# Performance work log

Hardware: AMD Instinct MI355X
Metric: run time of the kernel (lower is better)

The kernel has to match this reference:

```python
import jax, jax.numpy as jnp
import numpy as np

N_NODES = 50000
N_EDGES = 800000
N_GRAPHS = 64
F0 = 64          # num_features
HID = 512        # hidden_size
N_OUT = 1


def setup_inputs() -> dict:
    key = jax.random.key(0)
    ks = jax.random.split(key, 16)

    def p(k, shape, scale):
        return jax.random.normal(k, shape, jnp.float32) * scale

    inp = {}
    inp["feature"] = jax.random.normal(ks[0], (N_NODES, F0), jnp.float32)
    inp["edge_index"] = jax.random.randint(ks[1], (2, N_EDGES), 0, N_NODES)
    inp["protein_batch"] = jnp.sort(jax.random.randint(ks[2], (N_NODES,), 0, N_GRAPHS))

    dims = [(F0, F0), (F0, 2 * F0), (2 * F0, 4 * F0)]
    for i, (din, dout) in enumerate(dims):
        s = 1.0 / np.sqrt(din)
        inp[f"W{i+1}"] = p(ks[3 + 3 * i], (din, dout), s)      # GATConv lin weight
        inp[f"att{i+1}"] = p(ks[4 + 3 * i], (2, dout), 0.1)    # [att_src; att_dst]
        inp[f"b{i+1}"] = jnp.zeros((dout,), jnp.float32)       # GATConv bias
    inp["fc1_w"] = p(ks[12], (4 * F0, HID), 1.0 / np.sqrt(4 * F0))
    inp["fc1_b"] = jnp.zeros((HID,), jnp.float32)
    inp["fc2_w"] = p(ks[13], (HID, N_OUT), 1.0 / np.sqrt(HID))
    inp["fc2_b"] = jnp.zeros((N_OUT,), jnp.float32)
    return inp


def _gat_conv(x, src, dst, W, att, b):
    """PyG GATConv, heads=1, concat=True, negative_slope=0.2 (self-loops already in src/dst)."""
    h = x @ W                                             # [N, Dout]
    # per-edge attention logit: a_src . h_j + a_dst . h_i
    alpha = jax.nn.leaky_relu(h @ att[0], 0.2 * 0 + 0.0)  # placeholder, replaced below
    logit = jax.nn.leaky_relu((h @ att[0])[src] + (h @ att[1])[dst], negative_slope=0.2)  # [E]
    # segment softmax over edges grouped by destination node
    m = jax.ops.segment_max(logit, dst, num_segments=N_NODES)      # [N]
    e = jnp.exp(logit - m[dst])                                    # [E]
    s = jax.ops.segment_sum(e, dst, num_segments=N_NODES)          # [N]
    coef = e / s[dst]                                              # [E]
    out = jax.ops.segment_sum(coef[:, None] * h[src], dst, num_segments=N_NODES)  # [N, Dout]
    return out + b


def reference(feature, edge_index, protein_batch,
              W1, att1, b1, W2, att2, b2, W3, att3, b3,
              fc1_w, fc1_b, fc2_w, fc2_b):
    loop = jnp.arange(N_NODES)
    src = jnp.concatenate([edge_index[0], loop])   # add_self_loops=True
    dst = jnp.concatenate([edge_index[1], loop])

    x = jax.nn.relu(_gat_conv(feature, src, dst, W1, att1, b1))
    x = jax.nn.relu(_gat_conv(x, src, dst, W2, att2, b2))
    x = jax.nn.relu(_gat_conv(x, src, dst, W3, att3, b3))

    # global mean pool per graph
    sums = jax.ops.segment_sum(x, protein_batch, num_segments=N_GRAPHS)          # [G, 4F]
    cnts = jax.ops.segment_sum(jnp.ones((N_NODES,), x.dtype), protein_batch,
                               num_segments=N_GRAPHS)                            # [G]
    gc = sums / jnp.maximum(cnts, 1.0)[:, None]

    gc = jax.nn.relu(gc @ fc1_w + fc1_b)   # dropout is identity at inference
    return gc @ fc2_w + fc2_b
```

## Files before the change

### kernel.cpp

```cpp
#include <hip/hip_runtime.h>
#include <hip/hip_bf16.h>

#define N_NODES 50000
#define N_EDGES 800000
#define E_TOT   850000
#define N_GRAPHS 64
#define HID 512
#define NBC 196
#define PB  304
#define EB  3321
#define WB  12500

typedef unsigned short u16;
typedef __attribute__((ext_vector_type(8))) short short8;
typedef __attribute__((ext_vector_type(4))) float floatx4;
typedef union { uint4 u; short8 s; } frag_u;

__device__ inline unsigned f2b(float x) {
    unsigned u = __float_as_uint(x);
    return (u + 0x7fffu + ((u >> 16) & 1u)) >> 16;
}
__device__ inline float b2f_lo(unsigned u) { return __uint_as_float(u << 16); }
__device__ inline float b2f_hi(unsigned u) { return __uint_as_float(u & 0xffff0000u); }

struct PrepDesc {
    const float* W[3];
    const float* att[3];
    float* wsd[3];
    u16* Wt[3];
};

__global__ __launch_bounds__(256) void prep_count_kernel(PrepDesc d,
                                                         const int* __restrict__ dst_e,
                                                         int* __restrict__ cnt,
                                                         int* __restrict__ order) {
    const int DIN[3]  = {64, 64, 128};
    const int DOUT[3] = {64, 128, 256};
    int b = blockIdx.x;
    if (b >= PB) {
        int e = (b - PB) * 256 + threadIdx.x;
        if (e >= E_TOT) return;
        int dd = (e < N_EDGES) ? dst_e[e] : (e - N_EDGES);
        order[e] = atomicAdd(&cnt[dd], 1);
        return;
    }
    if (b < 128) {
        int wg = (b * 256 + (int)threadIdx.x) >> 6;
        int lane = threadIdx.x & 63;
        int l = (wg < 128) ? 0 : (wg < 256) ? 1 : 2;
        int base = (l == 0) ? 0 : (l == 1) ? 128 : 256;
        int k = wg - base;
        int Din = DIN[l], Dout = DOUT[l];
        int half = (k >= Din) ? 1 : 0;
        int row = half ? (k - Din) : k;
        float s = 0.f;
        for (int j = lane; j < Dout; j += 64)
            s += d.W[l][(size_t)row * Dout + j] * d.att[l][half * Dout + j];
#pragma unroll
        for (int off = 32; off > 0; off >>= 1) s += __shfl_xor(s, off);
        if (lane == 0) d.wsd[l][k] = s;
    } else {
        int t = (b - 128) * 256 + (int)threadIdx.x;
        int l; int off;
        if (t < 4096)       { l = 0; off = t; }
        else if (t < 12288) { l = 1; off = t - 4096; }
        else if (t < 45056) { l = 2; off = t - 12288; }
        else return;
        int Din = DIN[l], Dout = DOUT[l];
        int row = off / Dout, j = off & (Dout - 1);
        d.Wt[l][(size_t)j * Din + row] = (u16)f2b(d.W[l][off]);
    }
}

__global__ __launch_bounds__(256) void scan_cvt_kernel(const int* __restrict__ cnt,
                                                       int* __restrict__ row_ptr,
                                                       int* __restrict__ blocksum,
                                                       const float* __restrict__ feature,
                                                       const float* __restrict__ wsd1,
                                                       u16* __restrict__ Fb,
                                                       float* __restrict__ lsld1) {
    if (blockIdx.x < NBC) {
        __shared__ int buf[256];
        int tid = threadIdx.x;
        int i = blockIdx.x * 256 + tid;
        int v = (i < N_NODES) ? cnt[i] : 0;
        buf[tid] = v;
        __syncthreads();
        for (int off = 1; off < 256; off <<= 1) {
            int t = (tid >= off) ? buf[tid - off] : 0;
            __syncthreads();
            buf[tid] += t;
            __syncthreads();
        }
        if (i < N_NODES) row_ptr[i] = buf[tid] - v;
        if (tid == 255) blocksum[blockIdx.x] = buf[255];
    } else {
        int wid = ((blockIdx.x - NBC) * 256 + (int)threadIdx.x) >> 6;
        int lane = threadIdx.x & 63;
        if (wid >= N_NODES) return;
        float h = feature[(size_t)wid * 64 + lane];
        float a0 = h * wsd1[lane];
        float a1 = h * wsd1[64 + lane];
#pragma unroll
        for (int off = 32; off > 0; off >>= 1) {
            a0 += __shfl_xor(a0, off);
            a1 += __shfl_xor(a1, off);
        }
        if (lane == 0) { lsld1[wid] = a0; lsld1[N_NODES + wid] = a1; }
        Fb[(size_t)wid * 64 + lane] = (u16)f2b(h);
    }
}

__global__ __launch_bounds__(256) void scan_block_kernel(const int* __restrict__ blocksum,
                                                         int* __restrict__ blockoff,
                                                         int* __restrict__ row_ptr2_last) {
    __shared__ int buf[256];
    int tid = threadIdx.x;
    int v = (tid < NBC) ? blocksum[tid] : 0;
    buf[tid] = v;
    __syncthreads();
    for (int off = 1; off < 256; off <<= 1) {
        int t = (tid >= off) ? buf[tid - off] : 0;
        __syncthreads();
        buf[tid] += t;
        __syncthreads();
    }
    blockoff[tid] = buf[tid] - v;
    if (tid == 255) *row_ptr2_last = buf[255];
}

__global__ __launch_bounds__(256) void fin_fill_kernel(const int* __restrict__ edge_index,
                                                       const int* __restrict__ row_ptr,
                                                       const int* __restrict__ blockoff,
                                                       const int* __restrict__ order,
                                                       int* __restrict__ col_idx,
                                                       int* __restrict__ row_ptr2) {
    if (blockIdx.x < NBC) {
        int i = blockIdx.x * 256 + threadIdx.x;
        if (i < N_NODES) row_ptr2[i] = row_ptr[i] + blockoff[blockIdx.x];
        return;
    }
    int e = (blockIdx.x - NBC) * 256 + threadIdx.x;
    if (e >= E_TOT) return;
    int s, d;
    if (e < N_EDGES) { s = edge_index[e]; d = edge_index[N_EDGES + e]; }
    else             { s = e - N_EDGES;   d = s; }
    col_idx[row_ptr[d] + blockoff[d >> 8] + order[e]] = s;
}

template <int NN, int KK>
__global__ __launch_bounds__(256) void sgemm_mfma_kernel(const u16* __restrict__ A,
                                                         const u16* __restrict__ Bt,
                                                         u16* __restrict__ C,
                                                         const float* __restrict__ bias,
                                                         const float* __restrict__ wsd_next,
                                                         float* __restrict__ lsld_next,
                                                         const int* __restrict__ batch,
                                                         float* __restrict__ gsum_pool,
                                                         int M) {
    constexpr int NT = 4;
    constexpr int KSTEPS = KK / 32;
    constexpr int CS = 72;
    __shared__ u16 cst[4][32 * CS];
    const int lane = threadIdx.x & 63;
    const int w = threadIdx.x >> 6;
    const int c = lane & 15;
    const int q = lane >> 4;
    const int bn = blockIdx.y * 64;
    const int r0 = blockIdx.x * 128 + w * 32;
    int ar0 = r0 + c;      if (ar0 > M - 1) ar0 = M - 1;
    int ar1 = r0 + 16 + c; if (ar1 > M - 1) ar1 = M - 1;
    const u16* __restrict__ Ap0 = A + (size_t)ar0 * KK + q * 8;
    const u16* __restrict__ Ap1 = A + (size_t)ar1 * KK + q * 8;
    floatx4 acc[2][NT];
#pragma unroll
    for (int i = 0; i < 2; ++i)
#pragma unroll
        for (int b = 0; b < NT; ++b) acc[i][b] = (floatx4){0.f, 0.f, 0.f, 0.f};
#pragma unroll
    for (int ks = 0; ks < KSTEPS; ++ks) {
        const int k0 = ks * 32;
        frag_u a0, a1, bf[NT];
        a0.u = *(const uint4*)(Ap0 + k0);
        a1.u = *(const uint4*)(Ap1 + k0);
#pragma unroll
        for (int b = 0; b < NT; ++b)
            bf[b].u = *(const uint4*)(Bt + (size_t)(bn + b * 16 + c) * KK + q * 8 + k0);
#pragma unroll
        for (int b = 0; b < NT; ++b) {
            acc[0][b] = __builtin_amdgcn_mfma_f32_16x16x32_bf16(a0.s, bf[b].s, acc[0][b], 0, 0, 0);
            acc[1][b] = __builtin_amdgcn_mfma_f32_16x16x32_bf16(a1.s, bf[b].s, acc[1][b], 0, 0, 0);
        }
    }

    if (gsum_pool) {
        float bsv[NT];
#pragma unroll
        for (int b = 0; b < NT; ++b) bsv[b] = bias[bn + b * 16 + c];
        const bool full = (r0 + 31 < M);
        const int rl = full ? (r0 + 31) : (M - 1);
        if (full && batch[r0] == batch[rl]) {
            const int gr = batch[r0];
#pragma unroll
            for (int b = 0; b < NT; ++b) {
                float s = 0.f;
#pragma unroll
                for (int i = 0; i < 2; ++i)
#pragma unroll
                    for (int g = 0; g < 4; ++g) s += fmaxf(acc[i][b][g] + bsv[b], 0.f);
                s += __shfl_xor(s, 16);
                s += __shfl_xor(s, 32);
                if (q == 0) atomicAdd(&gsum_pool[gr * 256 + bn + b * 16 + c], s);
            }
        } else {
#pragma unroll
            for (int i = 0; i < 2; ++i) {
                int curg = -1;
                float sb[NT] = {0.f, 0.f, 0.f, 0.f};
#pragma unroll
                for (int g = 0; g < 4; ++g) {
                    int r = r0 + i * 16 + q * 4 + g;
                    if (r < M) {
                        int gr = batch[r];
                        if (gr != curg) {
                            if (curg >= 0) {
#pragma unroll
                                for (int b = 0; b < NT; ++b) {
                                    atomicAdd(&gsum_pool[curg * 256 + bn + b * 16 + c], sb[b]);
                                    sb[b] = 0.f;
                                }
                            }
                            curg = gr;
                        }
#pragma unroll
                        for (int b = 0; b < NT; ++b) sb[b] += fmaxf(acc[i][b][g] + bsv[b], 0.f);
                    }
                }
                if (curg >= 0) {
#pragma unroll
                    for (int b = 0; b < NT; ++b)
                        atomicAdd(&gsum_pool[curg * 256 + bn + b * 16 + c], sb[b]);
                }
            }
        }
        return;
    }

    const bool has_next = (wsd_next != nullptr);
    u16* __restrict__ cb = cst[w];
    float ps[2][4] = {}, pd[2][4] = {};
#pragma unroll
    for (int b = 0; b < NT; ++b) {
        const int col = bn + b * 16 + c;
        const float bsv = bias[col];
        const float wsv = has_next ? wsd_next[col] : 0.f;
        const float wdv = has_next ? wsd_next[NN + col] : 0.f;
#pragma unroll
        for (int i = 0; i < 2; ++i) {
#pragma unroll
            for (int g = 0; g < 4; ++g) {
                float v = fmaxf(acc[i][b][g] + bsv, 0.f);
                cb[(i * 16 + q * 4 + g) * CS + b * 16 + c] = (u16)f2b(v);
                ps[i][g] += v * wsv;
                pd[i][g] += v * wdv;
            }
        }
    }
    if (has_next) {
#pragma unroll
        for (int i = 0; i < 2; ++i)
#pragma unroll
            for (int g = 0; g < 4; ++g) {
#pragma unroll
                for (int mm = 1; mm < 16; mm <<= 1) {
                    ps[i][g] += __shfl_xor(ps[i][g], mm);
                    pd[i][g] += __shfl_xor(pd[i][g], mm);
                }
            }
        if (c == 0) {
#pragma unroll
            for (int i = 0; i < 2; ++i)
#pragma unroll
                for (int g = 0; g < 4; ++g) {
                    int r = r0 + i * 16 + q * 4 + g;
                    if (r < M) {
                        atomicAdd(&lsld_next[r], ps[i][g]);
                        atomicAdd(&lsld_next[M + r], pd[i][g]);
                    }
                }
        }
    }
#pragma unroll
    for (int p = 0; p < 4; ++p) {
        int lr = p * 8 + (lane >> 3);
        int r = r0 + lr;
        if (r < M) {
            uint4 val = *(const uint4*)&cb[lr * CS + (lane & 7) * 8];
            *(uint4*)(C + (size_t)r * NN + bn + (lane & 7) * 8) = val;
        }
    }
}

template <int D>
__global__ __launch_bounds__(256) void gather_fused_kernel(const u16* __restrict__ X,
                                                           const float* __restrict__ lsld,
                                                           const int* __restrict__ row_ptr,
                                                           const int* __restrict__ col_idx,
                                                           u16* __restrict__ out) {
    constexpr int L = D / 8;
    constexpr int P = 64 / L;
    __shared__ float2 ec_all[4][64];
    int wid = (blockIdx.x * 256 + threadIdx.x) >> 6;
    int lane = threadIdx.x & 63;
    if (wid >= N_NODES) return;
    float2* __restrict__ ec = ec_all[threadIdx.x >> 6];
    const int start = row_ptr[wid];
    const int end = row_ptr[wid + 1];
    const int deg = end - start;
    const float ldi = lsld[N_NODES + wid];
    const float* __restrict__ ls = lsld;
    const int eslot = lane / L;
    const int fidx = lane % L;
    float a[8] = {0.f, 0.f, 0.f, 0.f, 0.f, 0.f, 0.f, 0.f};

    auto fma8 = [&](float cc, uint4 v) {
        a[0] += cc * b2f_lo(v.x); a[1] += cc * b2f_hi(v.x);
        a[2] += cc * b2f_lo(v.y); a[3] += cc * b2f_hi(v.y);
        a[4] += cc * b2f_lo(v.z); a[5] += cc * b2f_hi(v.z);
        a[6] += cc * b2f_lo(v.w); a[7] += cc * b2f_hi(v.w);
    };

    if (deg <= 64) {
        int srcl = 0;
        float l = -3.0e38f;
        if (lane < deg) {
            srcl = col_idx[start + lane];
            float t = ls[srcl] + ldi;
            l = (t > 0.f) ? t : 0.2f * t;
        }
        float m = l;
#pragma unroll
        for (int off = 32; off > 0; off >>= 1) m = fmaxf(m, __shfl_xor(m, off));
        float e = (lane < deg) ? __expf(l - m) : 0.f;
        float s = e;
#pragma unroll
        for (int off = 32; off > 0; off >>= 1) s += __shfl_xor(s, off);
        ec[lane] = make_float2(e / s, __int_as_float(srcl));

        const int nsteps = (deg + P - 1) / P;
        for (int g0 = 0; g0 < nsteps; g0 += 4) {
            float2 p[4]; uint4 v[4];
#pragma unroll
            for (int j = 0; j < 4; ++j) {
                int idx = (g0 + j) * P + eslot;
                bool valid = idx < deg;
                p[j] = ec[valid ? idx : 0];
                if (!valid) p[j].x = 0.f;
            }
#pragma unroll
            for (int j = 0; j < 4; ++j)
                v[j] = *(const uint4*)(X + (size_t)__float_as_int(p[j].y) * D + fidx * 8);
#pragma unroll
            for (int j = 0; j < 4; ++j) fma8(p[j].x, v[j]);
        }
    } else {
        float m = -3.0e38f;
        for (int e = start + lane; e < end; e += 64) {
            float t = ls[col_idx[e]] + ldi;
            t = (t > 0.f) ? t : 0.2f * t;
            m = fmaxf(m, t);
        }
#pragma unroll
        for (int off = 32; off > 0; off >>= 1) m = fmaxf(m, __shfl_xor(m, off));
        float ssum = 0.f;
        for (int e = start + lane; e < end; e += 64) {
            float t = ls[col_idx[e]] + ldi;
            t = (t > 0.f) ? t : 0.2f * t;
            ssum += __expf(t - m);
        }
#pragma unroll
        for (int off = 32; off > 0; off >>= 1) ssum += __shfl_xor(ssum, off);
        const float inv = 1.0f / ssum;
        for (int e0 = start; e0 < end; e0 += P) {
            int e = e0 + eslot;
            if (e < end) {
                int src = col_idx[e];
                float t = ls[src] + ldi;
                t = (t > 0.f) ? t : 0.2f * t;
                float cc = __expf(t - m) * inv;
                uint4 v = *(const uint4*)(X + (size_t)src * D + fidx * 8);
                fma8(cc, v);
            }
        }
    }
#pragma unroll
    for (int mm = L; mm < 64; mm <<= 1) {
#pragma unroll
        for (int i = 0; i < 8; ++i) a[i] += __shfl_xor(a[i], mm);
    }
    if (lane < L) {
        uint4 o;
        o.x = f2b(a[0]) | (f2b(a[1]) << 16);
        o.y = f2b(a[2]) | (f2b(a[3]) << 16);
        o.z = f2b(a[4]) | (f2b(a[5]) << 16);
        o.w = f2b(a[6]) | (f2b(a[7]) << 16);
        *(uint4*)(out + (size_t)wid * D + lane * 8) = o;
    }
}

__device__ inline int lower_bound_dev(const int* __restrict__ a, int n, int v) {
    int lo = 0, hi = n;
    while (lo < hi) { int mid = (lo + hi) >> 1; if (a[mid] < v) lo = mid + 1; else hi = mid; }
    return lo;
}

__global__ __launch_bounds__(256) void fc_kernel(const float* __restrict__ gsum,
                                                 const int* __restrict__ batch,
                                                 const float* __restrict__ w1,
                                                 const float* __restrict__ b1,
                                                 const float* __restrict__ w2,
                                                 const float* __restrict__ b2,
                                                 float* __restrict__ out) {
    __shared__ float gc[256];
    __shared__ float h1s[HID];
    __shared__ float red[256];
    __shared__ int s_cnt;
    int g = blockIdx.x;
    int tid = threadIdx.x;
    if (tid == 0)
        s_cnt = lower_bound_dev(batch, N_NODES, g + 1) - lower_bound_dev(batch, N_NODES, g);
    __syncthreads();
    float denom = fmaxf((float)s_cnt, 1.0f);
    gc[tid] = gsum[g * 256 + tid] / denom;
    __syncthreads();
#pragma unroll
    for (int jj = 0; jj < 2; ++jj) {
        int j = tid + jj * 256;
        float sum = b1[j];
        for (int k = 0; k < 256; ++k) sum += gc[k] * w1[k * HID + j];
        h1s[j] = (sum > 0.f) ? sum : 0.f;
    }
    __syncthreads();
    float acc = h1s[tid] * w2[tid] + h1s[tid + 256] * w2[tid + 256];
    red[tid] = acc;
    __syncthreads();
    for (int off = 128; off > 0; off >>= 1) {
        if (tid < off) red[tid] += red[tid + off];
        __syncthreads();
    }
    if (tid == 0) out[g] = red[0] + b2[0];
}

extern "C" void kernel_launch(void* const* d_in, const int* in_sizes, int n_in,
                              void* d_out, int out_size, void* d_ws, size_t ws_size,
                              hipStream_t stream) {
    const float* feature  = (const float*)d_in[0];
    const int*   edge_idx = (const int*)d_in[1];
    const int*   batch    = (const int*)d_in[2];
    const float* W1    = (const float*)d_in[3];
    const float* att1  = (const float*)d_in[4];
    const float* b1    = (const float*)d_in[5];
    const float* W2    = (const float*)d_in[6];
    const float* att2  = (const float*)d_in[7];
    const float* b2    = (const float*)d_in[8];
    const float* W3    = (const float*)d_in[9];
    const float* att3  = (const float*)d_in[10];
    const float* b3    = (const float*)d_in[11];
    const float* fc1_w = (const float*)d_in[12];
    const float* fc1_b = (const float*)d_in[13];
    const float* fc2_w = (const float*)d_in[14];
    const float* fc2_b = (const float*)d_in[15];
    float* out = (float*)d_out;

    char* w = (char*)d_ws;
    auto alloc = [&](size_t bytes) {
        char* p = w;
        w += (bytes + 255) & ~(size_t)255;
        return p;
    };
    u16* Fb    = (u16*)alloc((size_t)N_NODES * 64 * 2);
    u16* X1b   = (u16*)alloc((size_t)N_NODES * 64 * 2);
    u16* X2b   = (u16*)alloc((size_t)N_NODES * 128 * 2);
    u16* AGGb  = (u16*)alloc((size_t)N_NODES * 128 * 2);
    float* lsld1 = (float*)alloc((size_t)N_NODES * 2 * 4);
    char* zbase = w;
    int* cnt      = (int*)alloc((size_t)N_NODES * 4);
    float* gsum   = (float*)alloc(64 * 256 * 4);
    float* lsld23 = (float*)alloc((size_t)N_NODES * 4 * 4);
    size_t zbytes = (size_t)(w - zbase);
    float* lsld2 = lsld23;
    float* lsld3 = lsld23 + (size_t)N_NODES * 2;
    float* wsd1  = (float*)alloc(2 * 64 * 4);
    float* wsd2  = (float*)alloc(2 * 64 * 4);
    float* wsd3  = (float*)alloc(2 * 128 * 4);
    u16* Wt1   = (u16*)alloc(64 * 64 * 2);
    u16* Wt2   = (u16*)alloc(128 * 64 * 2);
    u16* Wt3   = (u16*)alloc(256 * 128 * 2);
    int* row_ptr  = (int*)alloc((size_t)N_NODES * 4);
    int* row_ptr2 = (int*)alloc((size_t)(N_NODES + 1) * 4);
    int* col_idx  = (int*)alloc((size_t)E_TOT * 4);
    int* order    = (int*)alloc((size_t)E_TOT * 4);
    int* blocksum = (int*)alloc(256 * 4);
    int* blockoff = (int*)alloc(256 * 4);

    hipMemsetAsync(zbase, 0, zbytes, stream);

    const int GB = (N_NODES + 127) / 128;

    PrepDesc pd;
    pd.W[0] = W1; pd.W[1] = W2; pd.W[2] = W3;
    pd.att[0] = att1; pd.att[1] = att2; pd.att[2] = att3;
    pd.wsd[0] = wsd1; pd.wsd[1] = wsd2; pd.wsd[2] = wsd3;
    pd.Wt[0] = Wt1; pd.Wt[1] = Wt2; pd.Wt[2] = Wt3;

    prep_count_kernel<<<PB + EB, 256, 0, stream>>>(pd, edge_idx + N_EDGES, cnt, order);
    scan_cvt_kernel<<<NBC + WB, 256, 0, stream>>>(cnt, row_ptr, blocksum, feature, wsd1, Fb, lsld1);
    scan_block_kernel<<<1, 256, 0, stream>>>(blocksum, blockoff, row_ptr2 + N_NODES);
    fin_fill_kernel<<<NBC + EB, 256, 0, stream>>>(edge_idx, row_ptr, blockoff, order, col_idx, row_ptr2);

    gather_fused_kernel<64><<<WB, 256, 0, stream>>>(Fb, lsld1, row_ptr2, col_idx, AGGb);
    sgemm_mfma_kernel<64, 64><<<dim3(GB, 1), 256, 0, stream>>>(AGGb, Wt1, X1b, b1, wsd2, lsld2, nullptr, nullptr, N_NODES);

    gather_fused_kernel<64><<<WB, 256, 0, stream>>>(X1b, lsld2, row_ptr2, col_idx, AGGb);
    sgemm_mfma_kernel<128, 64><<<dim3(GB, 2), 256, 0, stream>>>(AGGb, Wt2, X2b, b2, wsd3, lsld3, nullptr, nullptr, N_NODES);

    gather_fused_kernel<128><<<WB, 256, 0, stream>>>(X2b, lsld3, row_ptr2, col_idx, AGGb);
    sgemm_mfma_kernel<256, 128><<<dim3(GB, 4), 256, 0, stream>>>(AGGb, Wt3, nullptr, b3, nullptr, nullptr, batch, gsum, N_NODES);

    fc_kernel<<<N_GRAPHS, 256, 0, stream>>>(gsum, batch, fc1_w, fc1_b, fc2_w, fc2_b, out);
}
```

Baseline: 299.8 us.

## Fuse block scan into fill kernel and use two nodes per wave for D=64 gathers

Every block of the fill kernel now redoes the small 196-entry block-offset scan in shared memory, which removes the separate single-block scan launch and its blockoff buffer. A new gather2 kernel handles two destination nodes per 64-lane wave for the 64-wide feature layers, with 32 lanes per node covering 4 edges by 8 bf16 features. This is meant to reduce idle lanes and halve the number of waves for low-degree nodes. The cost is redundant scan work in every fill block and more shuffle reductions for the per-node sums.

Measured after the change: 289.8 us, median of 2. -3.4%, faster.

```diff
diff --git a/kernel.cpp b/kernel.cpp
--- a/kernel.cpp
+++ b/kernel.cpp
@@ -10,6 +10,7 @@
 #define PB  304
 #define EB  3321
 #define WB  12500
+#define WB2 6250
 
 typedef unsigned short u16;
 typedef __attribute__((ext_vector_type(8))) short short8;
@@ -111,10 +112,14 @@
     }
 }
 
-__global__ __launch_bounds__(256) void scan_block_kernel(const int* __restrict__ blocksum,
-                                                         int* __restrict__ blockoff,
-                                                         int* __restrict__ row_ptr2_last) {
+__global__ __launch_bounds__(256) void fin_fill_kernel(const int* __restrict__ edge_index,
+                                                       const int* __restrict__ row_ptr,
+                                                       const int* __restrict__ blocksum,
+                                                       const int* __restrict__ order,
+                                                       int* __restrict__ col_idx,
+                                                       int* __restrict__ row_ptr2) {
     __shared__ int buf[256];
+    __shared__ int boff[256];
     int tid = threadIdx.x;
     int v = (tid < NBC) ? blocksum[tid] : 0;
     buf[tid] = v;
@@ -125,27 +130,21 @@
         buf[tid] += t;
         __syncthreads();
     }
-    blockoff[tid] = buf[tid] - v;
-    if (tid == 255) *row_ptr2_last = buf[255];
-}
-
-__global__ __launch_bounds__(256) void fin_fill_kernel(const int* __restrict__ edge_index,
-                                                       const int* __restrict__ row_ptr,
-                                                       const int* __restrict__ blockoff,
-                                                       const int* __restrict__ order,
-                                                       int* __restrict__ col_idx,
-                                                       int* __restrict__ row_ptr2) {
+    boff[tid] = buf[tid] - v;
+    __syncthreads();
+
     if (blockIdx.x < NBC) {
-        int i = blockIdx.x * 256 + threadIdx.x;
-        if (i < N_NODES) row_ptr2[i] = row_ptr[i] + blockoff[blockIdx.x];
+        int i = blockIdx.x * 256 + tid;
+        if (i < N_NODES) row_ptr2[i] = row_ptr[i] + boff[blockIdx.x];
+        if (blockIdx.x == 0 && tid == NBC - 1) row_ptr2[N_NODES] = buf[tid];
         return;
     }
-    int e = (blockIdx.x - NBC) * 256 + threadIdx.x;
+    int e = (blockIdx.x - NBC) * 256 + tid;
     if (e >= E_TOT) return;
     int s, d;
     if (e < N_EDGES) { s = edge_index[e]; d = edge_index[N_EDGES + e]; }
     else             { s = e - N_EDGES;   d = s; }
-    col_idx[row_ptr[d] + blockoff[d >> 8] + order[e]] = s;
+    col_idx[row_ptr[d] + boff[d >> 8] + order[e]] = s;
 }
 
 template <int NN, int KK>
@@ -298,6 +297,113 @@
             uint4 val = *(const uint4*)&cb[lr * CS + (lane & 7) * 8];
             *(uint4*)(C + (size_t)r * NN + bn + (lane & 7) * 8) = val;
         }
+    }
+}
+
+__global__ __launch_bounds__(256) void gather2_kernel(const u16* __restrict__ X,
+                                                      const float* __restrict__ lsld,
+                                                      const int* __restrict__ row_ptr,
+                                                      const int* __restrict__ col_idx,
+                                                      u16* __restrict__ out) {
+    __shared__ float2 ec_all[4][64];
+    int gw = (blockIdx.x * 256 + threadIdx.x) >> 6;
+    int lane = threadIdx.x & 63;
+    int half = lane >> 5;
+    int hl = lane & 31;
+    int nid = gw * 2 + half;
+    if (nid >= N_NODES) return;
+    float2* __restrict__ ec = ec_all[threadIdx.x >> 6] + half * 32;
+    const int start = row_ptr[nid];
+    const int end = row_ptr[nid + 1];
+    const int deg = end - start;
+    const float ldi = lsld[N_NODES + nid];
+    const float* __restrict__ ls = lsld;
+    const int eslot = hl >> 3;
+    const int fidx = hl & 7;
+    float a[8] = {0.f, 0.f, 0.f, 0.f, 0.f, 0.f, 0.f, 0.f};
+
+    auto fma8 = [&](float cc, uint4 v) {
+        a[0] += cc * b2f_lo(v.x); a[1] += cc * b2f_hi(v.x);
+        a[2] += cc * b2f_lo(v.y); a[3] += cc * b2f_hi(v.y);
+        a[4] += cc * b2f_lo(v.z); a[5] += cc * b2f_hi(v.z);
+        a[6] += cc * b2f_lo(v.w); a[7] += cc * b2f_hi(v.w);
+    };
+
+    if (deg <= 32) {
+        int srcl = 0;
+        float l = -3.0e38f;
+        if (hl < deg) {
+            srcl = col_idx[start + hl];
+            float t = ls[srcl] + ldi;
+            l = (t > 0.f) ? t : 0.2f * t;
+        }
+        float m = l;
+#pragma unroll
+        for (int off = 16; off > 0; off >>= 1) m = fmaxf(m, __shfl_xor(m, off));
+        float e = (hl < deg) ? __expf(l - m) : 0.f;
+        float s = e;
+#pragma unroll
+        for (int off = 16; off > 0; off >>= 1) s += __shfl_xor(s, off);
+        ec[hl] = make_float2(e / s, __int_as_float(srcl));
+
+        const int nsteps = (deg + 3) >> 2;
+        for (int g0 = 0; g0 < nsteps; g0 += 4) {
+            float2 p[4]; uint4 v[4];
+#pragma unroll
+            for (int j = 0; j < 4; ++j) {
+                int idx = (g0 + j) * 4 + eslot;
+                bool valid = idx < deg;
+                p[j] = ec[valid ? idx : 0];
+                if (!valid) p[j].x = 0.f;
+            }
+#pragma unroll
+            for (int j = 0; j < 4; ++j)
+                v[j] = *(const uint4*)(X + (size_t)__float_as_int(p[j].y) * 64 + fidx * 8);
+#pragma unroll
+            for (int j = 0; j < 4; ++j) fma8(p[j].x, v[j]);
+        }
+    } else {
+        float m = -3.0e38f;
+        for (int e = start + hl; e < end; e += 32) {
+            float t = ls[col_idx[e]] + ldi;
+            t = (t > 0.f) ? t : 0.2f * t;
+            m = fmaxf(m, t);
+        }
+#pragma unroll
+        for (int off = 16; off > 0; off >>= 1) m = fmaxf(m, __shfl_xor(m, off));
+        float ssum = 0.f;
+        for (int e = start + hl; e < end; e += 32) {
+            float t = ls[col_idx[e]] + ldi;
+            t = (t > 0.f) ? t : 0.2f * t;
+            ssum += __expf(t - m);
+        }
+#pragma unroll
+        for (int off = 16; off > 0; off >>= 1) ssum += __shfl_xor(ssum, off);
+        const float inv = 1.0f / ssum;
+        for (int e0 = start; e0 < end; e0 += 4) {
+            int e = e0 + eslot;
+            if (e < end) {
+                int src = col_idx[e];
+                float t = ls[src] + ldi;
+                t = (t > 0.f) ? t : 0.2f * t;
+                float cc = __expf(t - m) * inv;
+                uint4 v = *(const uint4*)(X + (size_t)src * 64 + fidx * 8);
+                fma8(cc, v);
+            }
+        }
+    }
+#pragma unroll
+    for (int mm = 8; mm < 32; mm <<= 1) {
+#pragma unroll
+        for (int i = 0; i < 8; ++i) a[i] += __shfl_xor(a[i], mm);
+    }
+    if (hl < 8) {
+        uint4 o;
+        o.x = f2b(a[0]) | (f2b(a[1]) << 16);
+        o.y = f2b(a[2]) | (f2b(a[3]) << 16);
+        o.z = f2b(a[4]) | (f2b(a[5]) << 16);
+        o.w = f2b(a[6]) | (f2b(a[7]) << 16);
+        *(uint4*)(out + (size_t)nid * 64 + hl * 8) = o;
     }
 }
 
@@ -501,7 +607,6 @@
     int* col_idx  = (int*)alloc((size_t)E_TOT * 4);
     int* order    = (int*)alloc((size_t)E_TOT * 4);
     int* blocksum = (int*)alloc(256 * 4);
-    int* blockoff = (int*)alloc(256 * 4);
 
     hipMemsetAsync(zbase, 0, zbytes, stream);
 
@@ -515,13 +620,12 @@
 
     prep_count_kernel<<<PB + EB, 256, 0, stream>>>(pd, edge_idx + N_EDGES, cnt, order);
     scan_cvt_kernel<<<NBC + WB, 256, 0, stream>>>(cnt, row_ptr, blocksum, feature, wsd1, Fb, lsld1);
-    scan_block_kernel<<<1, 256, 0, stream>>>(blocksum, blockoff, row_ptr2 + N_NODES);
-    fin_fill_kernel<<<NBC + EB, 256, 0, stream>>>(edge_idx, row_ptr, blockoff, order, col_idx, row_ptr2);
-
-    gather_fused_kernel<64><<<WB, 256, 0, stream>>>(Fb, lsld1, row_ptr2, col_idx, AGGb);
+    fin_fill_kernel<<<NBC + EB, 256, 0, stream>>>(edge_idx, row_ptr, blocksum, order, col_idx, row_ptr2);
+
+    gather2_kernel<<<WB2, 256, 0, stream>>>(Fb, lsld1, row_ptr2, col_idx, AGGb);
     sgemm_mfma_kernel<64, 64><<<dim3(GB, 1), 256, 0, stream>>>(AGGb, Wt1, X1b, b1, wsd2, lsld2, nullptr, nullptr, N_NODES);
 
-    gather_fused_kernel<64><<<WB, 256, 0, stream>>>(X1b, lsld2, row_ptr2, col_idx, AGGb);
+    gather2_kernel<<<WB2, 256, 0, stream>>>(X1b, lsld2, row_ptr2, col_idx, AGGb);
     sgemm_mfma_kernel<128, 64><<<dim3(GB, 2), 256, 0, stream>>>(AGGb, Wt2, X2b, b2, wsd3, lsld3, nullptr, nullptr, N_NODES);
 
     gather_fused_kernel<128><<<WB, 256, 0, stream>>>(X2b, lsld3, row_ptr2, col_idx, AGGb);
```
